# Kernel tuning notes

Hardware: AMD Instinct MI355X
Metric: run time of the kernel (lower is better)

## Reference

```python
import jax, jax.numpy as jnp
import numpy as np

CONF_THRES = 0.25
IOU_THRES = 0.45
MAX_DET = 1000
MAX_WH = 4096.0   # class offset for per-class NMS (yolov5 trick)
TOPK = 2048       # pre-NMS candidate cap (fixed-shape stand-in for max_nms)


def _xywh2xyxy(b):
    cx, cy, w, h = b[..., 0], b[..., 1], b[..., 2], b[..., 3]
    return jnp.stack([cx - w * 0.5, cy - h * 0.5, cx + w * 0.5, cy + h * 0.5], axis=-1)


def _box_iou(a, b):
    # a, b: [K, 4] in xyxy -> [K, K] pairwise IoU
    lt = jnp.maximum(a[:, None, :2], b[None, :, :2])
    rb = jnp.minimum(a[:, None, 2:], b[None, :, 2:])
    wh = jnp.clip(rb - lt, 0.0)
    inter = wh[..., 0] * wh[..., 1]
    area_a = (a[:, 2] - a[:, 0]) * (a[:, 3] - a[:, 1])
    area_b = (b[:, 2] - b[:, 0]) * (b[:, 3] - b[:, 1])
    return inter / (area_a[:, None] + area_b[None, :] - inter + 1e-7)


def _nms_single(pred):
    # pred: [N, 5+C] = (cx, cy, w, h, obj, cls...)
    obj = pred[:, 4]
    cls_prob = pred[:, 5:]
    cls_conf = jnp.max(cls_prob, axis=-1)
    cls_id = jnp.argmax(cls_prob, axis=-1)
    score = obj * cls_conf                      # conf = obj_conf * cls_conf (best class)
    valid = (obj > CONF_THRES) & (score > CONF_THRES)
    score = jnp.where(valid, score, 0.0)
    boxes = _xywh2xyxy(pred[:, :4])

    # keep top-K candidates by confidence (sorted descending)
    tops, idx = jax.lax.top_k(score, TOPK)
    boxes_k = boxes[idx]                        # [K, 4]
    cls_k = cls_id[idx]                         # [K]
    val_k = tops > 0.0

    # per-class NMS via class offset
    shifted = boxes_k + (cls_k.astype(boxes_k.dtype) * MAX_WH)[:, None]
    iou = _box_iou(shifted, shifted)            # [K, K]

    j = jnp.arange(TOPK)

    def body(i, keep):
        # if box i survives, suppress lower-scored boxes with IoU > thresh
        sup = keep[i] & (iou[i] > IOU_THRES) & (j > i)
        return keep & ~sup

    keep = jax.lax.fori_loop(0, TOPK, body, val_k)

    # gather up to MAX_DET kept detections (already score-sorted)
    fs, fi = jax.lax.top_k(jnp.where(keep, tops, -1.0), MAX_DET)
    ok = fs > 0.0
    det_boxes = jnp.where(ok[:, None], boxes_k[fi], 0.0)
    det_score = jnp.where(ok, tops[fi], 0.0)
    det_cls = jnp.where(ok, cls_k[fi].astype(det_boxes.dtype), -1.0)
    # [MAX_DET, 6] = (x1, y1, x2, y2, conf, cls); padded rows have conf 0, cls -1
    return jnp.concatenate([det_boxes, det_score[:, None], det_cls[:, None]], axis=-1)


def setup_inputs() -> dict:
    key = jax.random.key(0)
    raw = jax.random.uniform(key, (16, 25200, 85), dtype=jnp.float32)
    xy = raw[..., 0:2] * 640.0            # centers within a 640x640 image
    wh = raw[..., 2:4] * 120.0 + 2.0      # box sizes in [2, 122]
    rest = raw[..., 4:]                   # obj + class probs in [0, 1)
    pred = jnp.concatenate([xy, wh, rest], axis=-1)
    return {"pred": pred}


def reference(pred):
    return jax.vmap(_nms_single)(pred)
```

## Files before the change

kernel.cpp:

```cpp
#include <hip/hip_runtime.h>
#include <stdint.h>

#pragma clang fp contract(off)

#define BB 16
#define NN 25200
#define ROW 85
#define NCLS 80
#define TK 2048
#define SORTN 4096
#define NBIN 4096
#define MAXDET 1000
#define CONF 0.25f
#define IOUT 0.45f
#define SROWS 64
#define STH 0x3E800000u

typedef float fvec4 __attribute__((ext_vector_type(4)));

#define AS1 __attribute__((address_space(1)))
#define AS3 __attribute__((address_space(3)))

__global__ __launch_bounds__(128) void score_kernel(const float* __restrict__ pred,
                                                    float* __restrict__ scores,
                                                    uint8_t* __restrict__ cls,
                                                    unsigned int* __restrict__ hist) {
  __shared__ __align__(16) float srow[SROWS * ROW];
  const int tile = blockIdx.x;
  const int b = blockIdx.y;
  const int tid = threadIdx.x;
  const int lane = tid & 63;
  const int row0 = tile * SROWS;
  int nrows = NN - row0;
  if (nrows > SROWS) nrows = SROWS;
  const char* gsrc = (const char*)(pred + ((size_t)b * NN + row0) * ROW);
  const int nbytes = nrows * ROW * 4;
  for (int off = tid * 16; off < nbytes; off += 128 * 16) {
    __builtin_amdgcn_global_load_lds((AS1 void*)(gsrc + off),
                                     (AS3 void*)((char*)srow + (off - lane * 16)),
                                     16, 0, 0);
  }
  __builtin_amdgcn_s_waitcnt(0);
  __syncthreads();
  if (tid < nrows) {
    const int n = row0 + tid;
    const float* r = srow + tid * ROW;
    float obj = r[4];
    float best = r[5];
    int bid = 0;
#pragma unroll
    for (int c = 1; c < NCLS; ++c) {
      float p = r[5 + c];
      if (p > best) { best = p; bid = c; }
    }
    float score = obj * best;
    bool valid = (obj > CONF) && (score > CONF);
    float sout = valid ? score : 0.0f;
    scores[(size_t)b * NN + n] = sout;
    cls[(size_t)b * NN + n] = (uint8_t)bid;
    if (valid) {
      unsigned int u = __float_as_uint(sout);
      unsigned int bin = (u - (STH + 1u)) >> 12;
      if (bin > NBIN - 1) bin = NBIN - 1;
      atomicAdd(&hist[(size_t)b * NBIN + bin], 1u);
    }
  }
}

__global__ __launch_bounds__(256) void scan_kernel(const unsigned int* __restrict__ hist,
                                                   unsigned int* __restrict__ gsoff,
                                                   unsigned int* __restrict__ gcnt,
                                                   int* __restrict__ gP,
                                                   int* __restrict__ gtot) {
  const int b = blockIdx.x;
  const int t = threadIdx.x;
  const int w = t >> 6, lane = t & 63;
  for (int i = t; i < NBIN; i += 256) gcnt[(size_t)b * NBIN + i] = 0u;
  const unsigned int* h = hist + (size_t)b * NBIN;
  unsigned int loc[16];
  int ssum = 0;
#pragma unroll
  for (int k = 0; k < 16; ++k) {
    loc[k] = h[NBIN - 1 - (16 * t + k)];
    ssum += (int)loc[k];
  }
  int v = ssum;
  for (int o = 1; o < 64; o <<= 1) { int u = __shfl_up(v, o); if (lane >= o) v += u; }
  __shared__ int sw[4];
  __shared__ int sfound;
  if (t == 0) sfound = 0;
  if (lane == 63) sw[w] = v;
  __syncthreads();
  int wbase = 0;
  for (int i = 0; i < w; ++i) wbase += sw[i];
  const int total = sw[0] + sw[1] + sw[2] + sw[3];
  int run = wbase + v - ssum;
#pragma unroll
  for (int k = 0; k < 16; ++k) {
    int bin = NBIN - 1 - (16 * t + k);
    gsoff[(size_t)b * NBIN + bin] = (unsigned int)run;
    int c = (int)loc[k];
    if (run < TK && run + c >= TK) {
      gP[b] = bin;
      gtot[b] = run + c;
      sfound = 1;
    }
    run += c;
  }
  __syncthreads();
  if (t == 0 && !sfound) { gP[b] = 0; gtot[b] = total; }
}

__global__ __launch_bounds__(1024) void scatter_kernel(const float* __restrict__ scores,
                                                       const unsigned int* __restrict__ gsoff,
                                                       const int* __restrict__ gP,
                                                       unsigned int* __restrict__ gcnt,
                                                       unsigned long long* __restrict__ gskey) {
  const int b = blockIdx.y;
  const int n = blockIdx.x * 1024 + threadIdx.x;
  if (n >= NN) return;
  const unsigned int P = (unsigned int)gP[b];
  unsigned int u = __float_as_uint(scores[(size_t)b * NN + n]);
  if (u > STH) {
    unsigned int bin = (u - (STH + 1u)) >> 12;
    if (bin > NBIN - 1) bin = NBIN - 1;
    if (bin >= P) {
      unsigned int pos = gsoff[(size_t)b * NBIN + bin] +
                         atomicAdd(&gcnt[(size_t)b * NBIN + bin], 1u);
      if (pos < SORTN)
        gskey[(size_t)b * SORTN + pos] = ((unsigned long long)u << 32) | (unsigned int)(~n);
    }
  }
}

__global__ __launch_bounds__(1024) void emit_kernel(const float* __restrict__ pred,
                                                    const uint8_t* __restrict__ cls,
                                                    const unsigned int* __restrict__ gsoff,
                                                    const unsigned int* __restrict__ gcnt,
                                                    const unsigned long long* __restrict__ gskey,
                                                    const int* __restrict__ gtot,
                                                    float* __restrict__ gtops,
                                                    fvec4* __restrict__ gbox,
                                                    int* __restrict__ gcls) {
  const int b = blockIdx.y;
  const int stride = gridDim.x * 1024;
  const int tot = gtot[b];
  const int used = tot < SORTN ? tot : SORTN;
  const int npos = tot < TK ? tot : TK;
  for (int ip = npos + blockIdx.x * 1024 + threadIdx.x; ip < TK; ip += stride) {
    gtops[(size_t)b * TK + ip] = 0.0f;
    gcls[(size_t)b * TK + ip] = 0xFFFF;
    fvec4 z; z[0] = 0.f; z[1] = 0.f; z[2] = 0.f; z[3] = 0.f;
    gbox[(size_t)b * TK + ip] = z;
  }
  for (int pp = blockIdx.x * 1024 + threadIdx.x; pp < used; pp += stride) {
    unsigned long long k = gskey[(size_t)b * SORTN + pp];
    unsigned int u = (unsigned int)(k >> 32);
    unsigned int bin = (u - (STH + 1u)) >> 12;
    if (bin > NBIN - 1) bin = NBIN - 1;
    int base = (int)gsoff[(size_t)b * NBIN + bin];
    int cnt = (int)gcnt[(size_t)b * NBIN + bin];
    if (base + cnt > used) cnt = used - base;
    const unsigned long long* seg = gskey + (size_t)b * SORTN + base;
    int rank = 0;
    for (int j = 0; j < cnt; ++j) rank += (seg[j] > k) ? 1 : 0;
    int q = base + rank;
    if (q < npos) {
      int idx = (int)(~(unsigned int)k);
      gtops[(size_t)b * TK + q] = __uint_as_float(u);
      gcls[(size_t)b * TK + q] = (int)cls[(size_t)b * NN + idx];
      const float* rowp = pred + ((size_t)b * NN + idx) * ROW;
      float cx = rowp[0], cy = rowp[1], w2 = rowp[2], h2 = rowp[3];
      float hw = w2 * 0.5f, hh = h2 * 0.5f;
      fvec4 bb4;
      bb4[0] = cx - hw; bb4[1] = cy - hh; bb4[2] = cx + hw; bb4[3] = cy + hh;
      gbox[(size_t)b * TK + q] = bb4;
    }
  }
}

__global__ __launch_bounds__(64) void nms_kernel(const float* __restrict__ gtops,
                                                 const fvec4* __restrict__ gbox,
                                                 const int* __restrict__ gcls,
                                                 int* __restrict__ keep) {
  const int c = blockIdx.x;
  const int b = blockIdx.y;
  const int lane = threadIdx.x;
  __shared__ float sx1[TK], sy1[TK], sx2[TK], sy2[TK];
  __shared__ unsigned short spos[TK];
  __shared__ unsigned char skp[TK];

  int m = 0;
  for (int base = 0; base < TK; base += 64) {
    int j = base + lane;
    bool match = (gcls[(size_t)b * TK + j] == c);
    unsigned long long bal = __ballot(match);
    int mp = m + __popcll(bal & ((1ull << lane) - 1ull));
    if (match) {
      spos[mp] = (unsigned short)j;
      fvec4 bx = gbox[(size_t)b * TK + j];
      sx1[mp] = bx[0]; sy1[mp] = bx[1]; sx2[mp] = bx[2]; sy2[mp] = bx[3];
      skp[mp] = (gtops[(size_t)b * TK + j] > 0.0f) ? 1 : 0;
    }
    m += (int)__popcll(bal);
  }
  __syncthreads();

  for (int i = 0; i < m; ++i) {
    __syncthreads();
    if (!skp[i]) continue;
    float ax1 = sx1[i], ay1 = sy1[i], ax2 = sx2[i], ay2 = sy2[i];
    float aarea = (ax2 - ax1) * (ay2 - ay1);
    for (int j = i + 1 + lane; j < m; j += 64) {
      float bx1 = sx1[j], by1 = sy1[j], bx2 = sx2[j], by2 = sy2[j];
      float ltx = fmaxf(ax1, bx1), lty = fmaxf(ay1, by1);
      float rbx = fminf(ax2, bx2), rby = fminf(ay2, by2);
      float iw = fmaxf(rbx - ltx, 0.0f);
      float ih = fmaxf(rby - lty, 0.0f);
      float inter = iw * ih;
      float barea = (bx2 - bx1) * (by2 - by1);
      float iou = inter / (aarea + barea - inter + 1e-7f);
      if (iou > IOUT) skp[j] = 0;
    }
  }
  __syncthreads();

  for (int i = lane; i < m; i += 64) {
    keep[(size_t)b * TK + spos[i]] = skp[i];
  }
}

__global__ __launch_bounds__(256) void out_kernel(const float* __restrict__ gtops,
                                                  const fvec4* __restrict__ gbox,
                                                  const int* __restrict__ gcls,
                                                  const int* __restrict__ keep,
                                                  const int* __restrict__ gtot,
                                                  float* __restrict__ out) {
  int b = blockIdx.x;
  int t = threadIdx.x;
  __shared__ int scnt[256];
  int npos = gtot[b];
  if (npos > TK) npos = TK;
  const int CH = TK / 256;
  int base = t * CH;
  int kp[CH];
  int cnt = 0;
  for (int k = 0; k < CH; ++k) {
    int j = base + k;
    kp[k] = (j < npos) ? keep[(size_t)b * TK + j] : 0;
    cnt += kp[k];
  }
  scnt[t] = cnt;
  __syncthreads();
  for (int off = 1; off < 256; off <<= 1) {
    int v = (t >= off) ? scnt[t - off] : 0;
    __syncthreads();
    scnt[t] += v;
    __syncthreads();
  }
  int r = scnt[t] - cnt;
  int K = scnt[255];
  for (int k = 0; k < CH; ++k) {
    if (kp[k]) {
      if (r < MAXDET) {
        int j = base + k;
        float* o = out + ((size_t)b * MAXDET + r) * 6;
        fvec4 bx = gbox[(size_t)b * TK + j];
        o[0] = bx[0]; o[1] = bx[1]; o[2] = bx[2]; o[3] = bx[3];
        o[4] = gtops[(size_t)b * TK + j];
        o[5] = (float)gcls[(size_t)b * TK + j];
      }
      ++r;
    }
  }
  int Kc = K < MAXDET ? K : MAXDET;
  for (int r2 = Kc + t; r2 < MAXDET; r2 += 256) {
    float* o = out + ((size_t)b * MAXDET + r2) * 6;
    o[0] = 0.0f; o[1] = 0.0f; o[2] = 0.0f; o[3] = 0.0f; o[4] = 0.0f; o[5] = -1.0f;
  }
}

extern "C" void kernel_launch(void* const* d_in, const int* in_sizes, int n_in,
                              void* d_out, int out_size, void* d_ws, size_t ws_size,
                              hipStream_t stream) {
  const float* pred = (const float*)d_in[0];
  float* out = (float*)d_out;

  char* ws = (char*)d_ws;
  size_t off = 0;
  float*              scores = (float*)(ws + off);              off += (size_t)BB * NN * 4;
  uint8_t*            cls    = (uint8_t*)(ws + off);            off += (size_t)BB * NN;
  off = (off + 255) & ~(size_t)255;
  unsigned int*       hist   = (unsigned int*)(ws + off);       off += (size_t)BB * NBIN * 4;
  unsigned int*       gcnt   = (unsigned int*)(ws + off);       off += (size_t)BB * NBIN * 4;
  unsigned int*       gsoff  = (unsigned int*)(ws + off);       off += (size_t)BB * NBIN * 4;
  unsigned long long* gskey  = (unsigned long long*)(ws + off); off += (size_t)BB * SORTN * 8;
  float*              gtops  = (float*)(ws + off);              off += (size_t)BB * TK * 4;
  fvec4*              gbox   = (fvec4*)(ws + off);              off += (size_t)BB * TK * 16;
  int*                gcls   = (int*)(ws + off);                off += (size_t)BB * TK * 4;
  int*                keep   = (int*)(ws + off);                off += (size_t)BB * TK * 4;
  int*                gP     = (int*)(ws + off);                off += (size_t)BB * 4;
  int*                gtot   = (int*)(ws + off);                off += (size_t)BB * 4;
  (void)ws_size; (void)in_sizes; (void)n_in; (void)out_size;

  hipMemsetAsync(hist, 0, (size_t)BB * NBIN * 4, stream);
  score_kernel<<<dim3((NN + SROWS - 1) / SROWS, BB), 128, 0, stream>>>(pred, scores, cls, hist);
  scan_kernel<<<BB, 256, 0, stream>>>(hist, gsoff, gcnt, gP, gtot);
  scatter_kernel<<<dim3((NN + 1023) / 1024, BB), 1024, 0, stream>>>(scores, gsoff, gP, gcnt, gskey);
  emit_kernel<<<dim3(SORTN / 1024, BB), 1024, 0, stream>>>(pred, cls, gsoff, gcnt, gskey, gtot,
                                                           gtops, gbox, gcls);
  nms_kernel<<<dim3(NCLS, BB), 64, 0, stream>>>(gtops, gbox, gcls, keep);
  out_kernel<<<BB, 256, 0, stream>>>(gtops, gbox, gcls, keep, gtot, out);
}
```

Measured before the change: 260.5 us.

## Shrink NMS shared memory with register/LDS/global box tiers and drop per-iteration barrier

The per-class NMS kernel no longer stages all 2048 boxes in LDS. The first 64 are held in registers and broadcast by shuffle, the next ones up to 256 sit in small LDS arrays, and the rest are read from global memory. This cuts LDS use so more blocks fit per CU. The per-iteration __syncthreads is removed because a single wavefront runs the block, and already-suppressed candidates are skipped. The gcnt zeroing moves out of the scan kernel into a widened memset, which relies on gcnt sitting directly after hist in the workspace.

Measured after the change: 247.3 us. 5.1% less time.

```diff
diff --git a/kernel.cpp b/kernel.cpp
--- a/kernel.cpp
+++ b/kernel.cpp
@@ -15,6 +15,7 @@
 #define IOUT 0.45f
 #define SROWS 64
 #define STH 0x3E800000u
+#define MCAP 256
 
 typedef float fvec4 __attribute__((ext_vector_type(4)));
 
@@ -69,13 +70,11 @@
 
 __global__ __launch_bounds__(256) void scan_kernel(const unsigned int* __restrict__ hist,
                                                    unsigned int* __restrict__ gsoff,
-                                                   unsigned int* __restrict__ gcnt,
                                                    int* __restrict__ gP,
                                                    int* __restrict__ gtot) {
   const int b = blockIdx.x;
   const int t = threadIdx.x;
   const int w = t >> 6, lane = t & 63;
-  for (int i = t; i < NBIN; i += 256) gcnt[(size_t)b * NBIN + i] = 0u;
   const unsigned int* h = hist + (size_t)b * NBIN;
   unsigned int loc[16];
   int ssum = 0;
@@ -186,8 +185,8 @@
   const int c = blockIdx.x;
   const int b = blockIdx.y;
   const int lane = threadIdx.x;
-  __shared__ float sx1[TK], sy1[TK], sx2[TK], sy2[TK];
   __shared__ unsigned short spos[TK];
+  __shared__ float mx1[MCAP], my1[MCAP], mx2[MCAP], my2[MCAP];
   __shared__ unsigned char skp[TK];
 
   int m = 0;
@@ -198,29 +197,50 @@
     int mp = m + __popcll(bal & ((1ull << lane) - 1ull));
     if (match) {
       spos[mp] = (unsigned short)j;
-      fvec4 bx = gbox[(size_t)b * TK + j];
-      sx1[mp] = bx[0]; sy1[mp] = bx[1]; sx2[mp] = bx[2]; sy2[mp] = bx[3];
       skp[mp] = (gtops[(size_t)b * TK + j] > 0.0f) ? 1 : 0;
+      if (mp < MCAP) {
+        fvec4 bx = gbox[(size_t)b * TK + j];
+        mx1[mp] = bx[0]; my1[mp] = bx[1]; mx2[mp] = bx[2]; my2[mp] = bx[3];
+      }
     }
     m += (int)__popcll(bal);
   }
   __syncthreads();
 
+  float b0x1 = 0.f, b0y1 = 0.f, b0x2 = 0.f, b0y2 = 0.f;
+  if (lane < m) { b0x1 = mx1[lane]; b0y1 = my1[lane]; b0x2 = mx2[lane]; b0y2 = my2[lane]; }
+  __syncthreads();
+
   for (int i = 0; i < m; ++i) {
-    __syncthreads();
     if (!skp[i]) continue;
-    float ax1 = sx1[i], ay1 = sy1[i], ax2 = sx2[i], ay2 = sy2[i];
+    float ax1, ay1, ax2, ay2;
+    if (i < 64) {
+      ax1 = __shfl(b0x1, i); ay1 = __shfl(b0y1, i);
+      ax2 = __shfl(b0x2, i); ay2 = __shfl(b0y2, i);
+    } else if (i < MCAP) {
+      ax1 = mx1[i]; ay1 = my1[i]; ax2 = mx2[i]; ay2 = my2[i];
+    } else {
+      fvec4 bx = gbox[(size_t)b * TK + spos[i]];
+      ax1 = bx[0]; ay1 = bx[1]; ax2 = bx[2]; ay2 = bx[3];
+    }
     float aarea = (ax2 - ax1) * (ay2 - ay1);
-    for (int j = i + 1 + lane; j < m; j += 64) {
-      float bx1 = sx1[j], by1 = sy1[j], bx2 = sx2[j], by2 = sy2[j];
-      float ltx = fmaxf(ax1, bx1), lty = fmaxf(ay1, by1);
-      float rbx = fminf(ax2, bx2), rby = fminf(ay2, by2);
-      float iw = fmaxf(rbx - ltx, 0.0f);
-      float ih = fmaxf(rby - lty, 0.0f);
-      float inter = iw * ih;
-      float barea = (bx2 - bx1) * (by2 - by1);
-      float iou = inter / (aarea + barea - inter + 1e-7f);
-      if (iou > IOUT) skp[j] = 0;
+    for (int q = 0; q * 64 < m; ++q) {
+      int j = q * 64 + lane;
+      if (j > i && j < m && skp[j]) {
+        float jx1, jy1, jx2, jy2;
+        if (q == 0) { jx1 = b0x1; jy1 = b0y1; jx2 = b0x2; jy2 = b0y2; }
+        else if (j < MCAP) { jx1 = mx1[j]; jy1 = my1[j]; jx2 = mx2[j]; jy2 = my2[j]; }
+        else { fvec4 bx = gbox[(size_t)b * TK + spos[j]];
+               jx1 = bx[0]; jy1 = bx[1]; jx2 = bx[2]; jy2 = bx[3]; }
+        float ltx = fmaxf(ax1, jx1), lty = fmaxf(ay1, jy1);
+        float rbx = fminf(ax2, jx2), rby = fminf(ay2, jy2);
+        float iw = fmaxf(rbx - ltx, 0.0f);
+        float ih = fmaxf(rby - lty, 0.0f);
+        float inter = iw * ih;
+        float barea = (jx2 - jx1) * (jy2 - jy1);
+        float iou = inter / (aarea + barea - inter + 1e-7f);
+        if (iou > IOUT) skp[j] = 0;
+      }
     }
   }
   __syncthreads();
@@ -303,9 +323,9 @@
   int*                gtot   = (int*)(ws + off);                off += (size_t)BB * 4;
   (void)ws_size; (void)in_sizes; (void)n_in; (void)out_size;
 
-  hipMemsetAsync(hist, 0, (size_t)BB * NBIN * 4, stream);
+  hipMemsetAsync(hist, 0, (size_t)BB * NBIN * 4 * 2, stream);
   score_kernel<<<dim3((NN + SROWS - 1) / SROWS, BB), 128, 0, stream>>>(pred, scores, cls, hist);
-  scan_kernel<<<BB, 256, 0, stream>>>(hist, gsoff, gcnt, gP, gtot);
+  scan_kernel<<<BB, 256, 0, stream>>>(hist, gsoff, gP, gtot);
   scatter_kernel<<<dim3((NN + 1023) / 1024, BB), 1024, 0, stream>>>(scores, gsoff, gP, gcnt, gskey);
   emit_kernel<<<dim3(SORTN / 1024, BB), 1024, 0, stream>>>(pred, cls, gsoff, gcnt, gskey, gtot,
                                                            gtops, gbox, gcls);
```
